# Optimization experiments

Hardware: AMD Instinct MI355X
Metric: run time of the kernel (lower is better)

## Reference

```python
import jax, jax.numpy as jnp
import numpy as np

L, D_MODEL, D_INNER, DT_RANK, D_STATE, D_CONV, VOCAB = 4, 768, 1536, 48, 16, 4, 32000
B, S = 1, 1024


def rmsnorm(x, w, eps=1e-5):
    return x * jax.lax.rsqrt(jnp.mean(x * x, axis=-1, keepdims=True) + eps) * w


def causal_depthwise_conv(x, w, b):
    # x: [B,S,D]; w: [D,1,K] (torch Conv1d groups=D weight layout); causal left-pad K-1
    y = jax.lax.conv_general_dilated(
        x.transpose(0, 2, 1), w, window_strides=(1,), padding=[(D_CONV - 1, 0)],
        dimension_numbers=('NCH', 'OIH', 'NCH'), feature_group_count=D_INNER)
    return y.transpose(0, 2, 1) + b


def selective_scan(u, dt, A, Bm, Cm, Dv):
    # Faithful to the source: A_delta = exp(dt (x) A), clamp(min=-20) is a no-op on exp output
    A_delta = jnp.clip(jnp.exp(jnp.einsum('bld,dn->bldn', dt, A)), -20.0, None)
    B_delta_u = jnp.einsum('bld,bld,bln->bldn', dt, u, Bm)
    shifted = jnp.pad(A_delta[:, 1:], ((0, 0), (1, 0), (0, 0), (0, 0)))
    A_cum = jnp.exp(jnp.cumsum(shifted, axis=1))
    h = B_delta_u / (A_cum + 1e-12)
    y = jnp.einsum('bldn,bln->bld', jnp.cumsum(h, axis=1) * A_cum, Cm)
    return y + u * Dv


def setup_inputs() -> dict:
    key = jax.random.key(0)
    ks = jax.random.split(key, 8)
    return {
        'tokens': jax.random.randint(ks[0], (B, S), 0, VOCAB),
        'embedding': jax.random.normal(ks[1], (VOCAB, D_MODEL), jnp.float32) * 0.02,
        'norm_w': jnp.ones((L, D_MODEL), jnp.float32),
        'in_proj_w': jax.random.normal(ks[2], (L, 2 * D_INNER, D_MODEL), jnp.float32) * 0.02,
        'conv_w': jax.random.normal(ks[3], (L, D_INNER, 1, D_CONV), jnp.float32) * 0.2,
        'conv_b': jnp.zeros((L, D_INNER), jnp.float32),
        'x_proj_w': jax.random.normal(ks[4], (L, DT_RANK + 2 * D_STATE, D_INNER), jnp.float32) * 0.02,
        'dt_proj_w': jax.random.normal(ks[5], (L, D_INNER, DT_RANK), jnp.float32) * 0.001,
        'dt_proj_b': jnp.full((L, D_INNER), 5.0, jnp.float32),  # delta~5 keeps exp(cumsum(exp(dt*A))) finite
        'A_log': jnp.tile(jnp.log(jnp.arange(1, D_STATE + 1, dtype=jnp.float32)), (L, D_INNER, 1)),
        'D_skip': jnp.ones((L, D_INNER), jnp.float32),
        'out_proj_w': jax.random.normal(ks[6], (L, D_MODEL, D_INNER), jnp.float32) * 0.02,
        'final_norm_w': jnp.ones((D_MODEL,), jnp.float32),
    }


def reference(tokens, embedding, norm_w, in_proj_w, conv_w, conv_b, x_proj_w,
              dt_proj_w, dt_proj_b, A_log, D_skip, out_proj_w, final_norm_w):
    x = embedding[tokens]  # [B,S,d_model]
    for i in range(L):
        h = rmsnorm(x, norm_w[i])
        xz = h @ in_proj_w[i].T                      # [B,S,2*d_inner]
        xi, res = xz[..., :D_INNER], xz[..., D_INNER:]
        xi = jax.nn.silu(causal_depthwise_conv(xi, conv_w[i], conv_b[i]))
        proj = xi @ x_proj_w[i].T                    # [B,S,dt_rank+2*d_state]
        dt = jax.nn.softplus(proj[..., :DT_RANK] @ dt_proj_w[i].T + dt_proj_b[i])
        Bm = proj[..., DT_RANK:DT_RANK + D_STATE]
        Cm = proj[..., DT_RANK + D_STATE:]
        A = -jnp.exp(A_log[i])                       # [d_inner, d_state]
        y = selective_scan(xi, dt, A, Bm, Cm, D_skip[i])
        x = x + (y * jax.nn.silu(res)) @ out_proj_w[i].T
    return rmsnorm(x, final_norm_w) @ embedding.T    # tied LM head: [B,S,vocab]
```

## Files before the change

kernel.cpp:

```cpp
#include <hip/hip_runtime.h>
#include <hip/hip_bf16.h>
#include <cmath>

namespace {

constexpr int kL      = 4;
constexpr int kDModel = 768;
constexpr int kDInner = 1536;
constexpr int kDtRank = 48;
constexpr int kDState = 16;
constexpr int kDConv  = 4;
constexpr int kSeq    = 1024;
constexpr int kPLd    = 96;
constexpr int kPB     = 128;
constexpr int kVocab  = 32000;
constexpr int kCH     = 64;
constexpr int kNCH    = kSeq / kCH;
constexpr int kDN     = kDInner * kDState;
constexpr int kSplitIn  = 4;
constexpr int kSplitOut = 8;

constexpr int kPrepEmbed   = kSeq;
constexpr int kPrepF2b     = kVocab * kDModel / (8 * 256);
constexpr int kPrepDup2    = kL * kDModel * (kDInner / 4) / 256;
constexpr int kPrepSplit3  = kL * 2 * kDInner * (kDModel / 4) / 256;
constexpr int kPrepSplit3x = kL * kPB * (kDInner / 4) / 256;
constexpr int kPrepBlocks  = kPrepEmbed + kPrepF2b + kPrepDup2 + kPrepSplit3 + kPrepSplit3x;

using short8 = __attribute__((ext_vector_type(8))) short;
using f32x4  = __attribute__((ext_vector_type(4))) float;

__device__ __forceinline__ float silu_f(float v) {
    return v / (1.f + __expf(-v));
}

__device__ __forceinline__ unsigned short f2bu(float v) {
    __hip_bfloat16 h = __float2bfloat16(v);
    return *reinterpret_cast<unsigned short*>(&h);
}

__device__ __forceinline__ void split_bf16(float v, __hip_bfloat16& hi, __hip_bfloat16& lo) {
    hi = __float2bfloat16(v);
    lo = __float2bfloat16(v - __bfloat162float(hi));
}

__device__ __forceinline__ void split_u(float v, unsigned short& hi, unsigned short& lo) {
    __hip_bfloat16 h, l;
    split_bf16(v, h, l);
    hi = *reinterpret_cast<unsigned short*>(&h);
    lo = *reinterpret_cast<unsigned short*>(&l);
}

__global__ void __launch_bounds__(256) prep_kernel(
    const int* __restrict__ tokens, const float* __restrict__ embedding,
    const float* __restrict__ norm_w, const float* __restrict__ in_proj_w,
    const float* __restrict__ out_proj_w, const float* __restrict__ x_proj_w,
    float* __restrict__ x, __hip_bfloat16* __restrict__ h2,
    __hip_bfloat16* __restrict__ emb_bf, __hip_bfloat16* __restrict__ inw2,
    __hip_bfloat16* __restrict__ outw2, __hip_bfloat16* __restrict__ xw2) {
    const int tid = threadIdx.x;
    int b = blockIdx.x;

    if (b < kPrepEmbed) {
        const int s = b;
        const int t = tokens[s];
        const float* src = embedding + (size_t)t * kDModel;
        float v[3];
        float ss = 0.f;
        #pragma unroll
        for (int j = 0; j < 3; ++j) {
            const int d = tid + j * 256;
            v[j] = src[d];
            x[(size_t)s * kDModel + d] = v[j];
            ss = fmaf(v[j], v[j], ss);
        }
        #pragma unroll
        for (int m = 32; m; m >>= 1) ss += __shfl_xor(ss, m);
        __shared__ float red[4];
        if ((tid & 63) == 0) red[tid >> 6] = ss;
        __syncthreads();
        const float total = red[0] + red[1] + red[2] + red[3];
        const float scale = rsqrtf(total / (float)kDModel + 1e-5f);
        __hip_bfloat16* dst = h2 + (size_t)s * 3 * kDModel;
        #pragma unroll
        for (int j = 0; j < 3; ++j) {
            const int d = tid + j * 256;
            const float hv = v[j] * scale * norm_w[d];
            __hip_bfloat16 hi, lo;
            split_bf16(hv, hi, lo);
            dst[d] = hi; dst[kDModel + d] = lo; dst[2 * kDModel + d] = hi;
        }
        return;
    }
    b -= kPrepEmbed;

    if (b < kPrepF2b) {
        const int i = (b * 256 + tid) * 8;
        const float4 a = *reinterpret_cast<const float4*>(embedding + i);
        const float4 c = *reinterpret_cast<const float4*>(embedding + i + 4);
        union { unsigned short u[8]; uint4 v; } pk;
        pk.u[0] = f2bu(a.x); pk.u[1] = f2bu(a.y); pk.u[2] = f2bu(a.z); pk.u[3] = f2bu(a.w);
        pk.u[4] = f2bu(c.x); pk.u[5] = f2bu(c.y); pk.u[6] = f2bu(c.z); pk.u[7] = f2bu(c.w);
        *reinterpret_cast<uint4*>(reinterpret_cast<unsigned short*>(emb_bf) + i) = pk.v;
        return;
    }
    b -= kPrepF2b;

    if (b < kPrepDup2) {
        const int idx = b * 256 + tid;
        constexpr int cols = kDInner, c4cnt = kDInner / 4;
        const int r = idx / c4cnt, c = (idx % c4cnt) << 2;
        const float4 v = *reinterpret_cast<const float4*>(out_proj_w + (size_t)r * cols + c);
        ushort4 hi4 = {f2bu(v.x), f2bu(v.y), f2bu(v.z), f2bu(v.w)};
        unsigned short* row = reinterpret_cast<unsigned short*>(outw2) + (size_t)r * 2 * cols;
        *reinterpret_cast<ushort4*>(row + c) = hi4;
        *reinterpret_cast<ushort4*>(row + cols + c) = hi4;
        return;
    }
    b -= kPrepDup2;

    if (b < kPrepSplit3) {
        const int idx = b * 256 + tid;
        constexpr int cols = kDModel, c4cnt = kDModel / 4;
        const int r = idx / c4cnt, c = (idx % c4cnt) << 2;
        const float4 v = *reinterpret_cast<const float4*>(in_proj_w + (size_t)r * cols + c);
        ushort4 hi4, lo4;
        split_u(v.x, hi4.x, lo4.x); split_u(v.y, hi4.y, lo4.y);
        split_u(v.z, hi4.z, lo4.z); split_u(v.w, hi4.w, lo4.w);
        unsigned short* row = reinterpret_cast<unsigned short*>(inw2) + (size_t)r * 3 * cols;
        *reinterpret_cast<ushort4*>(row + c) = hi4;
        *reinterpret_cast<ushort4*>(row + cols + c) = hi4;
        *reinterpret_cast<ushort4*>(row + 2 * cols + c) = lo4;
        return;
    }
    b -= kPrepSplit3;

    {
        const int idx = b * 256 + tid;
        constexpr int c4cnt = kDInner / 4;
        const int layer = idx / (kPB * c4cnt);
        const int rem   = idx % (kPB * c4cnt);
        const int r = rem / c4cnt, c = (rem % c4cnt) << 2;
        float4 v = {0.f, 0.f, 0.f, 0.f};
        if (r < kDtRank + 2 * kDState)
            v = *reinterpret_cast<const float4*>(
                x_proj_w + (size_t)layer * (kDtRank + 2 * kDState) * kDInner + (size_t)r * kDInner + c);
        ushort4 hi4, lo4;
        split_u(v.x, hi4.x, lo4.x); split_u(v.y, hi4.y, lo4.y);
        split_u(v.z, hi4.z, lo4.z); split_u(v.w, hi4.w, lo4.w);
        unsigned short* row = reinterpret_cast<unsigned short*>(xw2)
            + ((size_t)layer * kPB + r) * 3 * kDInner;
        *reinterpret_cast<ushort4*>(row + c) = hi4;
        *reinterpret_cast<ushort4*>(row + kDInner + c) = hi4;
        *reinterpret_cast<ushort4*>(row + 2 * kDInner + c) = lo4;
    }
}

template <bool FINAL>
__global__ void __launch_bounds__(256) reduce_rms_kernel(
    const float* __restrict__ parts, size_t stride,
    const float* __restrict__ w, float* __restrict__ x,
    __hip_bfloat16* __restrict__ out) {
    const int s = blockIdx.x;
    float v[3];
    float ss = 0.f;
    #pragma unroll
    for (int j = 0; j < 3; ++j) {
        const int d = threadIdx.x + j * 256;
        const size_t off = (size_t)s * kDModel + d;
        float acc = x[off];
        #pragma unroll
        for (int p = 0; p < kSplitOut; ++p) acc += parts[(size_t)p * stride + off];
        v[j] = acc;
        x[off] = acc;
        ss = fmaf(acc, acc, ss);
    }
    #pragma unroll
    for (int m = 32; m; m >>= 1) ss += __shfl_xor(ss, m);
    __shared__ float red[4];
    if ((threadIdx.x & 63) == 0) red[threadIdx.x >> 6] = ss;
    __syncthreads();
    const float total = red[0] + red[1] + red[2] + red[3];
    const float scale = rsqrtf(total / (float)kDModel + 1e-5f);
    #pragma unroll
    for (int j = 0; j < 3; ++j) {
        const int d = threadIdx.x + j * 256;
        const float hv = v[j] * scale * w[d];
        if (FINAL) {
            out[(size_t)s * kDModel + d] = __float2bfloat16(hv);
        } else {
            __hip_bfloat16 hi, lo;
            split_bf16(hv, hi, lo);
            __hip_bfloat16* dst = out + (size_t)s * 3 * kDModel;
            dst[d] = hi; dst[kDModel + d] = lo; dst[2 * kDModel + d] = hi;
        }
    }
}

template <int BM, int BN, int KSPLIT>
__global__ void __launch_bounds__(256) mfma_gemm(
    const __hip_bfloat16* __restrict__ A, int lda,
    const __hip_bfloat16* __restrict__ B, int ldb,
    float* __restrict__ C, int ldc,
    int N, int K, size_t partStride) {
    constexpr int BK = 32;
    static_assert(BM == 128 && BN == 128, "staging assumes 128x128");
    __shared__ unsigned short As[2][BM * BK];
    __shared__ unsigned short Bs[2][BN * BK];
    const int tid  = threadIdx.x;
    const int lane = tid & 63;

    const int nwg = gridDim.x * gridDim.y;
    int bid = blockIdx.y * gridDim.x + blockIdx.x;
    {
        const int q = nwg >> 3, r = nwg & 7;
        const int xcd = bid & 7, pos = bid >> 3;
        bid = (xcd < r ? xcd * (q + 1) : r * (q + 1) + (xcd - r) * q) + pos;
    }
    const int m0 = (bid % gridDim.x) * BM;
    const int n0 = (bid / gridDim.x) * BN;

    const int Kp = K / KSPLIT;
    const int kbeg = (KSPLIT > 1) ? blockIdx.z * Kp : 0;
    float* Cw = (KSPLIT > 1) ? C + (size_t)blockIdx.z * partStride : C;
    constexpr int WM = BM / 2, WN = BN / 2;
    constexpr int MR = WM / 16, NR = WN / 16;
    const int wave = tid >> 6;
    const int wm = (wave >> 1) * WM, wn = (wave & 1) * WN;
    const int l15 = lane & 15, l4 = lane >> 4;
    f32x4 acc[MR][NR] = {};

    auto stage = [&](int buf, int k0) {
        #pragma unroll
        for (int i = 0; i < 2; ++i) {
            const int idx = tid + i * 256;
            const int r = idx >> 2, qv = idx & 3;
            const int qs = qv ^ ((r >> 1) & 3);
            __builtin_amdgcn_global_load_lds(
                (const __attribute__((address_space(1))) void*)(A + (size_t)(m0 + r) * lda + k0 + qs * 8),
                (__attribute__((address_space(3))) void*)(&As[buf][(idx - lane) * 8]),
                16, 0, 0);
        }
        #pragma unroll
        for (int i = 0; i < 2; ++i) {
            const int idx = tid + i * 256;
            const int r = idx >> 2, qv = idx & 3;
            const int qs = qv ^ ((r >> 1) & 3);
            __builtin_amdgcn_global_load_lds(
                (const __attribute__((address_space(1))) void*)(B + (size_t)(n0 + r) * ldb + k0 + qs * 8),
                (__attribute__((address_space(3))) void*)(&Bs[buf][(idx - lane) * 8]),
                16, 0, 0);
        }
    };

    const int nt = Kp / BK;
    int cur = 0;
    stage(0, kbeg);
    for (int t = 0; t < nt; ++t) {
        if (t + 1 < nt) {
            stage(cur ^ 1, kbeg + (t + 1) * BK);
            asm volatile("s_waitcnt vmcnt(4)" ::: "memory");
        } else {
            asm volatile("s_waitcnt vmcnt(0)" ::: "memory");
        }
        __builtin_amdgcn_s_barrier();

        short8 af[MR], bfv[NR];
        #pragma unroll
        for (int mi = 0; mi < MR; ++mi) {
            const int R = wm + mi * 16 + l15;
            af[mi] = *reinterpret_cast<const short8*>(&As[cur][(R * 4 + (l4 ^ ((R >> 1) & 3))) * 8]);
        }
        #pragma unroll
        for (int ni = 0; ni < NR; ++ni) {
            const int R = wn + ni * 16 + l15;
            bfv[ni] = *reinterpret_cast<const short8*>(&Bs[cur][(R * 4 + (l4 ^ ((R >> 1) & 3))) * 8]);
        }
        #pragma unroll
        for (int mi = 0; mi < MR; ++mi)
            #pragma unroll
            for (int ni = 0; ni < NR; ++ni)
                acc[mi][ni] = __builtin_amdgcn_mfma_f32_16x16x32_bf16(
                    af[mi], bfv[ni], acc[mi][ni], 0, 0, 0);

        asm volatile("s_waitcnt lgkmcnt(0)" ::: "memory");
        __builtin_amdgcn_s_barrier();
        cur ^= 1;
    }

    #pragma unroll
    for (int mi = 0; mi < MR; ++mi) {
        const int mrow = m0 + wm + mi * 16 + l4 * 4;
        #pragma unroll
        for (int ni = 0; ni < NR; ++ni) {
            const int ncol = n0 + wn + ni * 16 + l15;
            if (ncol >= N) continue;
            #pragma unroll
            for (int r = 0; r < 4; ++r)
                Cw[(size_t)(mrow + r) * ldc + ncol] = acc[mi][ni][r];
        }
    }
}

__global__ void __launch_bounds__(512) vocab_gemm(
    const __hip_bfloat16* __restrict__ A,
    const __hip_bfloat16* __restrict__ B,
    float* __restrict__ C) {
    constexpr int BM = 256, BN = 256, BK = 64;
    constexpr int K = kDModel, NT = K / BK;
    constexpr int lda = kDModel, ldb = kDModel, ldc = kVocab;
    extern __shared__ unsigned short lds[];
    unsigned short* AsB = lds;
    unsigned short* BsB = lds + 2 * BM * BK;
    const int tid = threadIdx.x, lane = tid & 63;
    const int wave = tid >> 6;
    const int wr = wave >> 2;
    const int wc = wave & 3;
    const int l15 = lane & 15, l4 = lane >> 4;

    const int nwg = gridDim.x * gridDim.y;
    int bid = blockIdx.y * gridDim.x + blockIdx.x;
    {
        const int q = nwg >> 3, r = nwg & 7;
        const int xcd = bid & 7, pos = bid >> 3;
        bid = (xcd < r ? xcd * (q + 1) : r * (q + 1) + (xcd - r) * q) + pos;
    }
    const int m0 = (bid % gridDim.x) * BM;
    const int n0 = (bid / gridDim.x) * BN;

    f32x4 acc[8][4] = {};

    auto stage = [&](int buf, int k0) {
        #pragma unroll
        for (int i = 0; i < 4; ++i) {
            const int idx = tid + i * 512;
            const int r = idx >> 3, p = idx & 7;
            const int ps = p ^ (r & 7);
            __builtin_amdgcn_global_load_lds(
                (const __attribute__((address_space(1))) void*)(A + (size_t)(m0 + r) * lda + k0 + ps * 8),
                (__attribute__((address_space(3))) void*)(AsB + (size_t)buf * BM * BK + (size_t)(idx - lane) * 8),
                16, 0, 0);
        }
        #pragma unroll
        for (int i = 0; i < 4; ++i) {
            const int idx = tid + i * 512;
            const int r = idx >> 3, p = idx & 7;
            const int ps = p ^ (r & 7);
            __builtin_amdgcn_global_load_lds(
                (const __attribute__((address_space(1))) void*)(B + (size_t)(n0 + r) * ldb + k0 + ps * 8),
                (__attribute__((address_space(3))) void*)(BsB + (size_t)buf * BN * BK + (size_t)(idx - lane) * 8),
                16, 0, 0);
        }
    };

    stage(0, 0);
    for (int t = 0; t < NT; ++t) {
        asm volatile("s_waitcnt vmcnt(0)" ::: "memory");
        __builtin_amdgcn_s_barrier();
        if (t + 1 < NT) stage((t + 1) & 1, (t + 1) * BK);
        const unsigned short* Ab = AsB + (size_t)(t & 1) * BM * BK;
        const unsigned short* Bb = BsB + (size_t)(t & 1) * BN * BK;

        short8 af[4][2], bfv[2][2];

#define LOAD_A(MQ)                                                          \
        _Pragma("unroll")                                                   \
        for (int mi = 0; mi < 4; ++mi) {                                    \
            _Pragma("unroll")                                               \
            for (int kk = 0; kk < 2; ++kk) {                                \
                const int R = wr * 128 + (MQ) * 64 + mi * 16 + l15;         \
                const int ps = (kk * 4 + l4) ^ (R & 7);                     \
                af[mi][kk] = *reinterpret_cast<const short8*>(              \
                    Ab + ((size_t)R * 8 + ps) * 8);                         \
            }                                                               \
        }
#define LOAD_B(NQ)                                                          \
        _Pragma("unroll")                                                   \
        for (int ni = 0; ni < 2; ++ni) {                                    \
            _Pragma("unroll")                                               \
            for (int kk = 0; kk < 2; ++kk) {                                \
                const int R = wc * 64 + (NQ) * 32 + ni * 16 + l15;          \
                const int ps = (kk * 4 + l4) ^ (R & 7);                     \
                bfv[ni][kk] = *reinterpret_cast<const short8*>(             \
                    Bb + ((size_t)R * 8 + ps) * 8);                         \
            }                                                               \
        }
#define QUAD(MQ, NQ)                                                        \
        __builtin_amdgcn_s_setprio(1);                                      \
        _Pragma("unroll")                                                   \
        for (int mi = 0; mi < 4; ++mi)                                      \
            _Pragma("unroll")                                               \
            for (int ni = 0; ni < 2; ++ni)                                  \
                _Pragma("unroll")                                           \
                for (int kk = 0; kk < 2; ++kk)                              \
                    acc[(MQ) * 4 + mi][(NQ) * 2 + ni] =                     \
                        __builtin_amdgcn_mfma_f32_16x16x32_bf16(            \
                            af[mi][kk], bfv[ni][kk],                        \
                            acc[(MQ) * 4 + mi][(NQ) * 2 + ni], 0, 0, 0);    \
        __builtin_amdgcn_s_setprio(0);

        LOAD_A(0); LOAD_B(0);
        QUAD(0, 0);
        LOAD_B(1);
        QUAD(0, 1);
        LOAD_A(1);
        QUAD(1, 1);
        LOAD_B(0);
        QUAD(1, 0);
#undef LOAD_A
#undef LOAD_B
#undef QUAD
    }

    #pragma unroll
    for (int mg = 0; mg < 8; ++mg) {
        const int mrow = m0 + wr * 128 + mg * 16 + l4 * 4;
        #pragma unroll
        for (int ng = 0; ng < 4; ++ng) {
            const int ncol = n0 + wc * 64 + ng * 16 + l15;
            #pragma unroll
            for (int r = 0; r < 4; ++r)
                C[(size_t)(mrow + r) * ldc + ncol] = acc[mg][ng][r];
        }
    }
}

template <int NP>
__global__ void __launch_bounds__(256) reduce_parts(
    const float* __restrict__ parts, size_t stride,
    float* __restrict__ dst, int count) {
    const int i = (blockIdx.x * 256 + threadIdx.x) * 4;
    if (i >= count) return;
    float4 s = *reinterpret_cast<const float4*>(parts + i);
    #pragma unroll
    for (int p = 1; p < NP; ++p) {
        const float4 v = *reinterpret_cast<const float4*>(parts + (size_t)p * stride + i);
        s.x += v.x; s.y += v.y; s.z += v.z; s.w += v.w;
    }
    *reinterpret_cast<float4*>(dst + i) = s;
}

__global__ void __launch_bounds__(256) conv_silu_kernel(
    const float* __restrict__ parts, size_t stride,
    const float* __restrict__ cw, const float* __restrict__ cb,
    float* __restrict__ xi, __hip_bfloat16* __restrict__ xi2) {
    const int s = blockIdx.x;
    const int d = blockIdx.y * 256 + threadIdx.x;
    float acc = cb[d];
    #pragma unroll
    for (int k = 0; k < kDConv; ++k) {
        const int sl = s - (kDConv - 1) + k;
        if (sl >= 0) {
            const size_t off = (size_t)sl * (2 * kDInner) + d;
            float xzv = parts[off];
            #pragma unroll
            for (int p = 1; p < kSplitIn; ++p) xzv += parts[(size_t)p * stride + off];
            acc = fmaf(xzv, cw[d * kDConv + k], acc);
        }
    }
    const float v = silu_f(acc);
    xi[(size_t)s * kDInner + d] = v;
    __hip_bfloat16 hi, lo;
    split_bf16(v, hi, lo);
    __hip_bfloat16* row = xi2 + (size_t)s * 3 * kDInner;
    row[d] = hi; row[kDInner + d] = lo; row[2 * kDInner + d] = hi;
}

__device__ __forceinline__ void compute_dt_tile(
    const float* __restrict__ proj, const float* __restrict__ dtw,
    const float* __restrict__ dtb, int l0, int d0, int tid,
    float (*sP)[kDtRank], float (*sdtw)[kDtRank + 1], float (*sdt)[16]) {
    for (int idx = tid; idx < kCH * kDtRank; idx += 256) {
        const int r = idx / kDtRank, c = idx % kDtRank;
        sP[r][c] = proj[(size_t)(l0 + r) * kPLd + c];
    }
    for (int idx = tid; idx < 16 * kDtRank; idx += 256) {
        const int dd = idx / kDtRank, c = idx % kDtRank;
        sdtw[dd][c] = dtw[(size_t)(d0 + dd) * kDtRank + c];
    }
    __syncthreads();
    #pragma unroll
    for (int e = 0; e < 4; ++e) {
        const int idx = tid + e * 256;
        const int r = idx >> 4, dd = idx & 15;
        float acc = dtb[d0 + dd];
        #pragma unroll
        for (int k = 0; k < kDtRank; ++k)
            acc = fmaf(sP[r][k], sdtw[dd][k], acc);
        acc = (acc > 20.f) ? acc : log1pf(__expf(acc));
        sdt[r][dd] = acc;
    }
}

__global__ void __launch_bounds__(256) scan_part1(
    const float* __restrict__ u, const float* __restrict__ proj,
    const float* __restrict__ A_log, const float* __restrict__ dtw,
    const float* __restrict__ dtb,
    float* __restrict__ P, float* __restrict__ S) {
    __shared__ float sP[kCH][kDtRank];
    __shared__ float sdtw[16][kDtRank + 1];
    __shared__ float sdt[kCH][16], su[kCH][16], sB[kCH][16];
    const int tid = threadIdx.x;
    const int n = tid & 15, dl = tid >> 4;
    const int d0 = blockIdx.x * 16;
    const int l0 = blockIdx.y * kCH;
    for (int idx = tid; idx < kCH * 16; idx += 256) {
        const int r = idx >> 4, c = idx & 15;
        su[r][c] = u[(size_t)(l0 + r) * kDInner + d0 + c];
        sB[r][c] = proj[(size_t)(l0 + r) * kPLd + kDtRank + c];
    }
    compute_dt_tile(proj, dtw, dtb, l0, d0, tid, sP, sdtw, sdt);
    __syncthreads();
    const int d = d0 + dl;
    const float Adn = -__expf(A_log[d * kDState + n]);
    float state = 0.f, sumA = 0.f;
    #pragma unroll 8
    for (int l = 0; l < kCH; ++l) {
        const float dtv = sdt[l][dl];
        const float adelta = __expf(dtv * Adn);
        const float mult = __expf(adelta);
        state = fmaf(state, mult, dtv * su[l][dl] * sB[l][n]);
        sumA += adelta;
    }
    const int dn = d * kDState + n;
    P[(size_t)blockIdx.y * kDN + dn] = __expf(sumA);
    S[(size_t)blockIdx.y * kDN + dn] = state;
}

__global__ void __launch_bounds__(256) scan_part2(
    const float* __restrict__ u, const float* __restrict__ proj,
    const float* __restrict__ A_log, const float* __restrict__ dtw,
    const float* __restrict__ dtb, const float* __restrict__ D_skip,
    const float* __restrict__ P, const float* __restrict__ S,
    const float* __restrict__ resparts, size_t rstride,
    __hip_bfloat16* __restrict__ g2) {
    __shared__ float sP[kCH][kDtRank];
    __shared__ float sdtw[16][kDtRank + 1];
    __shared__ float sdt[kCH][16], su[kCH][16], sB[kCH][16], sC[kCH][16];
    __shared__ float sy[kCH][16];
    const int tid = threadIdx.x;
    const int n = tid & 15, dl = tid >> 4;
    const int d0 = blockIdx.x * 16;
    const int l0 = blockIdx.y * kCH;
    for (int idx = tid; idx < kCH * 16; idx += 256) {
        const int r = idx >> 4, c = idx & 15;
        su[r][c] = u[(size_t)(l0 + r) * kDInner + d0 + c];
        sB[r][c] = proj[(size_t)(l0 + r) * kPLd + kDtRank + c];
        sC[r][c] = proj[(size_t)(l0 + r) * kPLd + kDtRank + kDState + c];
    }
    compute_dt_tile(proj, dtw, dtb, l0, d0, tid, sP, sdtw, sdt);
    const int dn = d0 * kDState + tid;
    float state = 0.f;
    for (int jj = 0; jj < (int)blockIdx.y; ++jj) {
        const size_t idx = (size_t)jj * kDN + dn;
        state = fmaf(state, P[idx], S[idx]);
    }
    __syncthreads();
    const int d = d0 + dl;
    const float Adn = -__expf(A_log[d * kDState + n]);
    const float Dv  = D_skip[d];
    for (int l = 0; l < kCH; ++l) {
        const float dtv = sdt[l][dl];
        const float uv  = su[l][dl];
        const float mult = __expf(__expf(dtv * Adn));
        state = fmaf(state, mult, dtv * uv * sB[l][n]);
        float contrib = state * sC[l][n];
        contrib += __shfl_xor(contrib, 8);
        contrib += __shfl_xor(contrib, 4);
        contrib += __shfl_xor(contrib, 2);
        contrib += __shfl_xor(contrib, 1);
        if (n == 0) sy[l][dl] = fmaf(uv, Dv, contrib);
    }
    __syncthreads();
    for (int idx = tid; idx < kCH * 16; idx += 256) {
        const int r = idx >> 4, c = idx & 15;
        const size_t roff = (size_t)(l0 + r) * (2 * kDInner) + kDInner + d0 + c;
        float res = resparts[roff];
        #pragma unroll
        for (int p = 1; p < kSplitIn; ++p) res += resparts[(size_t)p * rstride + roff];
        const float v = sy[r][c] * silu_f(res);
        __hip_bfloat16 hi, lo;
        split_bf16(v, hi, lo);
        __hip_bfloat16* row = g2 + (size_t)(l0 + r) * 2 * kDInner;
        row[d0 + c] = hi; row[kDInner + d0 + c] = lo;
    }
}

}

extern "C" void kernel_launch(void* const* d_in, const int* in_sizes, int n_in,
                              void* d_out, int out_size, void* d_ws, size_t ws_size,
                              hipStream_t stream) {
    const int*   tokens       = (const int*)d_in[0];
    const float* embedding    = (const float*)d_in[1];
    const float* norm_w       = (const float*)d_in[2];
    const float* in_proj_w    = (const float*)d_in[3];
    const float* conv_w       = (const float*)d_in[4];
    const float* conv_b       = (const float*)d_in[5];
    const float* x_proj_w     = (const float*)d_in[6];
    const float* dt_proj_w    = (const float*)d_in[7];
    const float* dt_proj_b    = (const float*)d_in[8];
    const float* A_log        = (const float*)d_in[9];
    const float* D_skip       = (const float*)d_in[10];
    const float* out_proj_w   = (const float*)d_in[11];
    const float* final_norm_w = (const float*)d_in[12];
    float* out = (float*)d_out;

    constexpr int K3m = 3 * kDModel;
    constexpr int K3i = 3 * kDInner;
    constexpr int K2i = 2 * kDInner;

    (void)hipFuncSetAttribute((const void*)vocab_gemm,
                              hipFuncAttributeMaxDynamicSharedMemorySize, 131072);

    char* ws = (char*)d_ws;
    auto alloc = [&](size_t bytes) { char* p = ws; ws += (bytes + 255) & ~(size_t)255; return p; };
    float* x    = (float*)alloc((size_t)kSeq * kDModel * 4);
    float* xi   = (float*)alloc((size_t)kSeq * kDInner * 4);
    float* proj = (float*)alloc((size_t)kSeq * kPLd * 4);
    float* scanP  = (float*)alloc((size_t)kNCH * kDN * 4);
    float* scanS  = (float*)alloc((size_t)kNCH * kDN * 4);
    float* partsXZ = (float*)alloc((size_t)kSplitIn * kSeq * 2 * kDInner * 4);
    float* partsP  = (float*)alloc((size_t)24 * kSeq * kPLd * 4);
    float* partsO  = (float*)alloc((size_t)kSplitOut * kSeq * kDModel * 4);
    __hip_bfloat16* h_bf   = (__hip_bfloat16*)alloc((size_t)kSeq * kDModel * 2);
    __hip_bfloat16* h2     = (__hip_bfloat16*)alloc((size_t)kSeq * K3m * 2);
    __hip_bfloat16* xi2    = (__hip_bfloat16*)alloc((size_t)kSeq * K3i * 2);
    __hip_bfloat16* g2     = (__hip_bfloat16*)alloc((size_t)kSeq * K2i * 2);
    __hip_bfloat16* emb_bf = (__hip_bfloat16*)alloc((size_t)kVocab * kDModel * 2);
    __hip_bfloat16* inw2   = (__hip_bfloat16*)alloc((size_t)kL * 2 * kDInner * K3m * 2);
    __hip_bfloat16* outw2  = (__hip_bfloat16*)alloc((size_t)kL * kDModel * K2i * 2);
    __hip_bfloat16* xw2    = (__hip_bfloat16*)alloc((size_t)kL * kPB * K3i * 2);

    prep_kernel<<<kPrepBlocks, 256, 0, stream>>>(
        tokens, embedding, norm_w, in_proj_w, out_proj_w, x_proj_w,
        x, h2, emb_bf, inw2, outw2, xw2);

    for (int i = 0; i < kL; ++i) {
        mfma_gemm<128, 128, kSplitIn><<<dim3(kSeq / 128, 2 * kDInner / 128, kSplitIn), 256, 0, stream>>>(
            h2, K3m, inw2 + (size_t)i * 2 * kDInner * K3m, K3m,
            partsXZ, 2 * kDInner, 2 * kDInner, K3m, (size_t)kSeq * 2 * kDInner);

        conv_silu_kernel<<<dim3(kSeq, kDInner / 256), 256, 0, stream>>>(
            partsXZ, (size_t)kSeq * 2 * kDInner,
            conv_w + (size_t)i * kDInner * kDConv, conv_b + (size_t)i * kDInner,
            xi, xi2);

        mfma_gemm<128, 128, 24><<<dim3(kSeq / 128, 1, 24), 256, 0, stream>>>(
            xi2, K3i, xw2 + (size_t)i * kPB * K3i, K3i,
            partsP, kPLd, kPLd, K3i, (size_t)kSeq * kPLd);
        reduce_parts<24><<<(kSeq * kPLd / 4 + 255) / 256, 256, 0, stream>>>(
            partsP, (size_t)kSeq * kPLd, proj, kSeq * kPLd);

        const float* A_l  = A_log + (size_t)i * kDInner * kDState;
        const float* dtw  = dt_proj_w + (size_t)i * kDInner * kDtRank;
        const float* dtb  = dt_proj_b + (size_t)i * kDInner;
        scan_part1<<<dim3(kDInner / 16, kNCH), 256, 0, stream>>>(
            xi, proj, A_l, dtw, dtb, scanP, scanS);
        scan_part2<<<dim3(kDInner / 16, kNCH), 256, 0, stream>>>(
            xi, proj, A_l, dtw, dtb, D_skip + (size_t)i * kDInner,
            scanP, scanS, partsXZ, (size_t)kSeq * 2 * kDInner, g2);

        mfma_gemm<128, 128, kSplitOut><<<dim3(kSeq / 128, kDModel / 128, kSplitOut), 256, 0, stream>>>(
            g2, K2i, outw2 + (size_t)i * kDModel * K2i, K2i,
            partsO, kDModel, kDModel, K2i, (size_t)kSeq * kDModel);

        if (i + 1 < kL) {
            reduce_rms_kernel<false><<<kSeq, 256, 0, stream>>>(
                partsO, (size_t)kSeq * kDModel, norm_w + (size_t)(i + 1) * kDModel, x, h2);
        } else {
            reduce_rms_kernel<true><<<kSeq, 256, 0, stream>>>(
                partsO, (size_t)kSeq * kDModel, final_norm_w, x, h_bf);
        }
    }

    vocab_gemm<<<dim3(kSeq / 256, kVocab / 256), 512, 131072, stream>>>(
        h_bf, emb_bf, out);
}
```

Baseline: 730.8 us.

## Replace duplicated split-bf16 operand copies with K-index wraparound in GEMM staging

The split-precision GEMMs previously stored activations and weights with a duplicated third (or second) K segment so that a plain K loop produced hi*hi + lo*hi + hi*lo. The GEMM now takes per-operand wrap thresholds (TA/TB), and staging remaps k past the threshold back to the start. This lets the activation and weight buffers store only hi and lo halves, and lets out_proj store a single bf16 copy. The aim is to cut prep writes, buffer footprint and the global/cache traffic from duplicated data. The cost is two compares per staging step, and correctness depends on the K layout matching the remap exactly.

```diff
diff --git a/kernel.cpp b/kernel.cpp
--- a/kernel.cpp
+++ b/kernel.cpp
@@ -19,13 +19,14 @@
 constexpr int kDN     = kDInner * kDState;
 constexpr int kSplitIn  = 4;
 constexpr int kSplitOut = 8;
+constexpr int kNoRemap  = 1 << 28;
 
 constexpr int kPrepEmbed   = kSeq;
 constexpr int kPrepF2b     = kVocab * kDModel / (8 * 256);
-constexpr int kPrepDup2    = kL * kDModel * (kDInner / 4) / 256;
-constexpr int kPrepSplit3  = kL * 2 * kDInner * (kDModel / 4) / 256;
-constexpr int kPrepSplit3x = kL * kPB * (kDInner / 4) / 256;
-constexpr int kPrepBlocks  = kPrepEmbed + kPrepF2b + kPrepDup2 + kPrepSplit3 + kPrepSplit3x;
+constexpr int kPrepOutW    = kL * kDModel * kDInner / (8 * 256);
+constexpr int kPrepInW     = kL * 2 * kDInner * kDModel / (8 * 256);
+constexpr int kPrepXW      = kL * kPB * kDInner / (8 * 256);
+constexpr int kPrepBlocks  = kPrepEmbed + kPrepF2b + kPrepOutW + kPrepInW + kPrepXW;
 
 using short8 = __attribute__((ext_vector_type(8))) short;
 using f32x4  = __attribute__((ext_vector_type(4))) float;
@@ -49,6 +50,18 @@
     split_bf16(v, h, l);
     hi = *reinterpret_cast<unsigned short*>(&h);
     lo = *reinterpret_cast<unsigned short*>(&l);
+}
+
+__device__ __forceinline__ void split8(const float* __restrict__ src,
+                                       uint4& hiv, uint4& lov) {
+    const float4 a = *reinterpret_cast<const float4*>(src);
+    const float4 b = *reinterpret_cast<const float4*>(src + 4);
+    union { unsigned short u[8]; uint4 v; } H, L;
+    split_u(a.x, H.u[0], L.u[0]); split_u(a.y, H.u[1], L.u[1]);
+    split_u(a.z, H.u[2], L.u[2]); split_u(a.w, H.u[3], L.u[3]);
+    split_u(b.x, H.u[4], L.u[4]); split_u(b.y, H.u[5], L.u[5]);
+    split_u(b.z, H.u[6], L.u[6]); split_u(b.w, H.u[7], L.u[7]);
+    hiv = H.v; lov = L.v;
 }
 
 __global__ void __launch_bounds__(256) prep_kernel(
@@ -57,7 +70,7 @@
     const float* __restrict__ out_proj_w, const float* __restrict__ x_proj_w,
     float* __restrict__ x, __hip_bfloat16* __restrict__ h2,
     __hip_bfloat16* __restrict__ emb_bf, __hip_bfloat16* __restrict__ inw2,
-    __hip_bfloat16* __restrict__ outw2, __hip_bfloat16* __restrict__ xw2) {
+    __hip_bfloat16* __restrict__ outw, __hip_bfloat16* __restrict__ xw2) {
     const int tid = threadIdx.x;
     int b = blockIdx.x;
 
@@ -81,14 +94,14 @@
         __syncthreads();
         const float total = red[0] + red[1] + red[2] + red[3];
         const float scale = rsqrtf(total / (float)kDModel + 1e-5f);
-        __hip_bfloat16* dst = h2 + (size_t)s * 3 * kDModel;
+        __hip_bfloat16* dst = h2 + (size_t)s * 2 * kDModel;
         #pragma unroll
         for (int j = 0; j < 3; ++j) {
             const int d = tid + j * 256;
             const float hv = v[j] * scale * norm_w[d];
             __hip_bfloat16 hi, lo;
             split_bf16(hv, hi, lo);
-            dst[d] = hi; dst[kDModel + d] = lo; dst[2 * kDModel + d] = hi;
+            dst[d] = hi; dst[kDModel + d] = lo;
         }
         return;
     }
@@ -106,53 +119,45 @@
     }
     b -= kPrepF2b;
 
-    if (b < kPrepDup2) {
+    if (b < kPrepOutW) {
+        const int i = (b * 256 + tid) * 8;
+        const float4 a = *reinterpret_cast<const float4*>(out_proj_w + i);
+        const float4 c = *reinterpret_cast<const float4*>(out_proj_w + i + 4);
+        union { unsigned short u[8]; uint4 v; } pk;
+        pk.u[0] = f2bu(a.x); pk.u[1] = f2bu(a.y); pk.u[2] = f2bu(a.z); pk.u[3] = f2bu(a.w);
+        pk.u[4] = f2bu(c.x); pk.u[5] = f2bu(c.y); pk.u[6] = f2bu(c.z); pk.u[7] = f2bu(c.w);
+        *reinterpret_cast<uint4*>(reinterpret_cast<unsigned short*>(outw) + i) = pk.v;
+        return;
+    }
+    b -= kPrepOutW;
+
+    if (b < kPrepInW) {
         const int idx = b * 256 + tid;
-        constexpr int cols = kDInner, c4cnt = kDInner / 4;
-        const int r = idx / c4cnt, c = (idx % c4cnt) << 2;
-        const float4 v = *reinterpret_cast<const float4*>(out_proj_w + (size_t)r * cols + c);
-        ushort4 hi4 = {f2bu(v.x), f2bu(v.y), f2bu(v.z), f2bu(v.w)};
-        unsigned short* row = reinterpret_cast<unsigned short*>(outw2) + (size_t)r * 2 * cols;
-        *reinterpret_cast<ushort4*>(row + c) = hi4;
-        *reinterpret_cast<ushort4*>(row + cols + c) = hi4;
+        constexpr int cols = kDModel, c8 = kDModel / 8;
+        const int r = idx / c8, c = (idx % c8) * 8;
+        uint4 hiv, lov;
+        split8(in_proj_w + (size_t)r * cols + c, hiv, lov);
+        unsigned short* row = reinterpret_cast<unsigned short*>(inw2) + (size_t)r * 2 * cols;
+        *reinterpret_cast<uint4*>(row + c) = hiv;
+        *reinterpret_cast<uint4*>(row + cols + c) = lov;
         return;
     }
-    b -= kPrepDup2;
-
-    if (b < kPrepSplit3) {
-        const int idx = b * 256 + tid;
-        constexpr int cols = kDModel, c4cnt = kDModel / 4;
-        const int r = idx / c4cnt, c = (idx % c4cnt) << 2;
-        const float4 v = *reinterpret_cast<const float4*>(in_proj_w + (size_t)r * cols + c);
-        ushort4 hi4, lo4;
-        split_u(v.x, hi4.x, lo4.x); split_u(v.y, hi4.y, lo4.y);
-        split_u(v.z, hi4.z, lo4.z); split_u(v.w, hi4.w, lo4.w);
-        unsigned short* row = reinterpret_cast<unsigned short*>(inw2) + (size_t)r * 3 * cols;
-        *reinterpret_cast<ushort4*>(row + c) = hi4;
-        *reinterpret_cast<ushort4*>(row + cols + c) = hi4;
-        *reinterpret_cast<ushort4*>(row + 2 * cols + c) = lo4;
-        return;
-    }
-    b -= kPrepSplit3;
+    b -= kPrepInW;
 
     {
         const int idx = b * 256 + tid;
-        constexpr int c4cnt = kDInner / 4;
-        const int layer = idx / (kPB * c4cnt);
-        const int rem   = idx % (kPB * c4cnt);
-        const int r = rem / c4cnt, c = (rem % c4cnt) << 2;
-        float4 v = {0.f, 0.f, 0.f, 0.f};
+        constexpr int cols = kDInner, c8 = kDInner / 8;
+        const int layer = idx / (kPB * c8);
+        const int rem   = idx % (kPB * c8);
+        const int r = rem / c8, c = (rem % c8) * 8;
+        uint4 hiv = {0, 0, 0, 0}, lov = {0, 0, 0, 0};
         if (r < kDtRank + 2 * kDState)
-            v = *reinterpret_cast<const float4*>(
-                x_proj_w + (size_t)layer * (kDtRank + 2 * kDState) * kDInner + (size_t)r * kDInner + c);
-        ushort4 hi4, lo4;
-        split_u(v.x, hi4.x, lo4.x); split_u(v.y, hi4.y, lo4.y);
-        split_u(v.z, hi4.z, lo4.z); split_u(v.w, hi4.w, lo4.w);
+            split8(x_proj_w + (size_t)layer * (kDtRank + 2 * kDState) * cols
+                   + (size_t)r * cols + c, hiv, lov);
         unsigned short* row = reinterpret_cast<unsigned short*>(xw2)
-            + ((size_t)layer * kPB + r) * 3 * kDInner;
-        *reinterpret_cast<ushort4*>(row + c) = hi4;
-        *reinterpret_cast<ushort4*>(row + kDInner + c) = hi4;
-        *reinterpret_cast<ushort4*>(row + 2 * kDInner + c) = lo4;
+            + ((size_t)layer * kPB + r) * 2 * cols;
+        *reinterpret_cast<uint4*>(row + c) = hiv;
+        *reinterpret_cast<uint4*>(row + cols + c) = lov;
     }
 }
 
@@ -191,16 +196,16 @@
         } else {
             __hip_bfloat16 hi, lo;
             split_bf16(hv, hi, lo);
-            __hip_bfloat16* dst = out + (size_t)s * 3 * kDModel;
-            dst[d] = hi; dst[kDModel + d] = lo; dst[2 * kDModel + d] = hi;
+            __hip_bfloat16* dst = out + (size_t)s * 2 * kDModel;
+            dst[d] = hi; dst[kDModel + d] = lo;
         }
     }
 }
 
 template <int BM, int BN, int KSPLIT>
 __global__ void __launch_bounds__(256) mfma_gemm(
-    const __hip_bfloat16* __restrict__ A, int lda,
-    const __hip_bfloat16* __restrict__ B, int ldb,
+    const __hip_bfloat16* __restrict__ A, int lda, int TA,
+    const __hip_bfloat16* __restrict__ B, int ldb, int TB,
     float* __restrict__ C, int ldc,
     int N, int K, size_t partStride) {
     constexpr int BK = 32;
@@ -231,13 +236,15 @@
     f32x4 acc[MR][NR] = {};
 
     auto stage = [&](int buf, int k0) {
+        const int ka = (k0 >= TA) ? k0 - TA : k0;
+        const int kb = (k0 >= TB) ? k0 - TB : k0;
         #pragma unroll
         for (int i = 0; i < 2; ++i) {
             const int idx = tid + i * 256;
             const int r = idx >> 2, qv = idx & 3;
             const int qs = qv ^ ((r >> 1) & 3);
             __builtin_amdgcn_global_load_lds(
-                (const __attribute__((address_space(1))) void*)(A + (size_t)(m0 + r) * lda + k0 + qs * 8),
+                (const __attribute__((address_space(1))) void*)(A + (size_t)(m0 + r) * lda + ka + qs * 8),
                 (__attribute__((address_space(3))) void*)(&As[buf][(idx - lane) * 8]),
                 16, 0, 0);
         }
@@ -247,7 +254,7 @@
             const int r = idx >> 2, qv = idx & 3;
             const int qs = qv ^ ((r >> 1) & 3);
             __builtin_amdgcn_global_load_lds(
-                (const __attribute__((address_space(1))) void*)(B + (size_t)(n0 + r) * ldb + k0 + qs * 8),
+                (const __attribute__((address_space(1))) void*)(B + (size_t)(n0 + r) * ldb + kb + qs * 8),
                 (__attribute__((address_space(3))) void*)(&Bs[buf][(idx - lane) * 8]),
                 16, 0, 0);
         }
@@ -462,8 +469,8 @@
     xi[(size_t)s * kDInner + d] = v;
     __hip_bfloat16 hi, lo;
     split_bf16(v, hi, lo);
-    __hip_bfloat16* row = xi2 + (size_t)s * 3 * kDInner;
-    row[d] = hi; row[kDInner + d] = lo; row[2 * kDInner + d] = hi;
+    __hip_bfloat16* row = xi2 + (size_t)s * 2 * kDInner;
+    row[d] = hi; row[kDInner + d] = lo;
 }
 
 __device__ __forceinline__ void compute_dt_tile(
@@ -624,21 +631,22 @@
     float* partsP  = (float*)alloc((size_t)24 * kSeq * kPLd * 4);
     float* partsO  = (float*)alloc((size_t)kSplitOut * kSeq * kDModel * 4);
     __hip_bfloat16* h_bf   = (__hip_bfloat16*)alloc((size_t)kSeq * kDModel * 2);
-    __hip_bfloat16* h2     = (__hip_bfloat16*)alloc((size_t)kSeq * K3m * 2);
-    __hip_bfloat16* xi2    = (__hip_bfloat16*)alloc((size_t)kSeq * K3i * 2);
-    __hip_bfloat16* g2     = (__hip_bfloat16*)alloc((size_t)kSeq * K2i * 2);
+    __hip_bfloat16* h2     = (__hip_bfloat16*)alloc((size_t)kSeq * 2 * kDModel * 2);
+    __hip_bfloat16* xi2    = (__hip_bfloat16*)alloc((size_t)kSeq * 2 * kDInner * 2);
+    __hip_bfloat16* g2     = (__hip_bfloat16*)alloc((size_t)kSeq * 2 * kDInner * 2);
     __hip_bfloat16* emb_bf = (__hip_bfloat16*)alloc((size_t)kVocab * kDModel * 2);
-    __hip_bfloat16* inw2   = (__hip_bfloat16*)alloc((size_t)kL * 2 * kDInner * K3m * 2);
-    __hip_bfloat16* outw2  = (__hip_bfloat16*)alloc((size_t)kL * kDModel * K2i * 2);
-    __hip_bfloat16* xw2    = (__hip_bfloat16*)alloc((size_t)kL * kPB * K3i * 2);
+    __hip_bfloat16* inw2   = (__hip_bfloat16*)alloc((size_t)kL * 2 * kDInner * 2 * kDModel * 2);
+    __hip_bfloat16* outw   = (__hip_bfloat16*)alloc((size_t)kL * kDModel * kDInner * 2);
+    __hip_bfloat16* xw2    = (__hip_bfloat16*)alloc((size_t)kL * kPB * 2 * kDInner * 2);
 
     prep_kernel<<<kPrepBlocks, 256, 0, stream>>>(
         tokens, embedding, norm_w, in_proj_w, out_proj_w, x_proj_w,
-        x, h2, emb_bf, inw2, outw2, xw2);
+        x, h2, emb_bf, inw2, outw, xw2);
 
     for (int i = 0; i < kL; ++i) {
         mfma_gemm<128, 128, kSplitIn><<<dim3(kSeq / 128, 2 * kDInner / 128, kSplitIn), 256, 0, stream>>>(
-            h2, K3m, inw2 + (size_t)i * 2 * kDInner * K3m, K3m,
+            h2, 2 * kDModel, 2 * kDModel,
+            inw2 + (size_t)i * 2 * kDInner * 2 * kDModel, 2 * kDModel, kDModel,
             partsXZ, 2 * kDInner, 2 * kDInner, K3m, (size_t)kSeq * 2 * kDInner);
 
         conv_silu_kernel<<<dim3(kSeq, kDInner / 256), 256, 0, stream>>>(
@@ -647,7 +655,8 @@
             xi, xi2);
 
         mfma_gemm<128, 128, 24><<<dim3(kSeq / 128, 1, 24), 256, 0, stream>>>(
-            xi2, K3i, xw2 + (size_t)i * kPB * K3i, K3i,
+            xi2, 2 * kDInner, 2 * kDInner,
+            xw2 + (size_t)i * kPB * 2 * kDInner, 2 * kDInner, kDInner,
             partsP, kPLd, kPLd, K3i, (size_t)kSeq * kPLd);
         reduce_parts<24><<<(kSeq * kPLd / 4 + 255) / 256, 256, 0, stream>>>(
             partsP, (size_t)kSeq * kPLd, proj, kSeq * kPLd);
@@ -662,7 +671,8 @@
             scanP, scanS, partsXZ, (size_t)kSeq * 2 * kDInner, g2);
 
         mfma_gemm<128, 128, kSplitOut><<<dim3(kSeq / 128, kDModel / 128, kSplitOut), 256, 0, stream>>>(
-            g2, K2i, outw2 + (size_t)i * kDModel * K2i, K2i,
+            g2, 2 * kDInner, kNoRemap,
+            outw + (size_t)i * kDModel * kDInner, kDInner, kDInner,
             partsO, kDModel, kDModel, K2i, (size_t)kSeq * kDModel);
 
         if (i + 1 < kL) {
```

Result: no change. 721.9 us (-1.2%).
